# Kernel optimization log

Hardware: AMD Instinct MI355X
Metric: run time of the kernel (lower is better)

## Reference

```python
import jax, jax.numpy as jnp
import numpy as np

N_NODES = 100000
D = 256
E = 1000000
H = 128


def setup_inputs() -> dict:
    key = jax.random.key(0)
    k1, k2, k3, k4 = jax.random.split(key, 4)
    z = jax.random.normal(k1, (N_NODES, D), dtype=jnp.float32)
    edge_label_index = jax.random.randint(k2, (2, E), 0, N_NODES, dtype=jnp.int64)
    # Linear layers: PyTorch Linear(in, out) -> weight [out, in]; stored here as [in, out].
    W1 = jax.random.normal(k3, (2 * D, H), dtype=jnp.float32) * (1.0 / np.sqrt(2 * D))
    b1 = jnp.zeros((H,), dtype=jnp.float32)
    W2 = jax.random.normal(k4, (H, 1), dtype=jnp.float32) * (1.0 / np.sqrt(H))
    b2 = jnp.zeros((1,), dtype=jnp.float32)
    return {"z": z, "edge_label_index": edge_label_index,
            "W1": W1, "b1": b1, "W2": W2, "b2": b2}


def reference(z, edge_label_index, W1, b1, W2, b2):
    src = edge_label_index[0]
    dst = edge_label_index[1]
    # Gather node pairs and concat: [E, 2*D]
    pair = jnp.concatenate([z[src], z[dst]], axis=-1)
    h = jax.nn.relu(pair @ W1 + b1)          # [E, H]
    out = (h @ W2 + b2).reshape(-1)          # [E]
    return out
```

## Files before the change

### kernel.cpp

```cpp
#include <hip/hip_runtime.h>
#include <hip/hip_bf16.h>


typedef __attribute__((ext_vector_type(4))) float floatx4;
typedef __attribute__((ext_vector_type(8))) short short8;
typedef _Float16 half8v __attribute__((ext_vector_type(8)));
typedef __fp16 fp16x2 __attribute__((ext_vector_type(2)));

#if defined(__has_builtin)
#if __has_builtin(__builtin_amdgcn_fdot2)
#define HAVE_FDOT2 1
#endif
#endif

__device__ __forceinline__ unsigned short bf16rne(float x) {
    unsigned int u = __float_as_uint(x);
    u += 0x7fffu + ((u >> 16) & 1u);
    return (unsigned short)(u >> 16);
}

__device__ __forceinline__ void gl_lds16(const void* g, void* l) {
    __builtin_amdgcn_global_load_lds(
        (const __attribute__((address_space(1))) void*)(unsigned long long)g,
        (__attribute__((address_space(3))) void*)(unsigned)(unsigned long long)l,
        16, 0, 0);
}

__global__ void cvt_w1h(const float* __restrict__ W1, unsigned short* __restrict__ BTc2) {
    int t = blockIdx.x * blockDim.x + threadIdx.x;
    int hf = t >> 15, rem = t & 32767;
    int s = rem >> 12, rem2 = rem & 4095;
    int n = rem2 >> 5, rem3 = rem2 & 31;
    int gp = rem3 >> 3, j = rem3 & 7;
    int g = gp ^ ((n >> 1) & 3);
    int k = hf * 256 + s * 32 + g * 8 + j;
    BTc2[t] = bf16rne(W1[k * 128 + n]);
}

__global__ void cvt_w1(const float* __restrict__ W1, unsigned short* __restrict__ BTc) {
    int t = blockIdx.x * blockDim.x + threadIdx.x;
    int s = t >> 12, rem = t & 4095;
    int n = rem >> 5, rem2 = rem & 31;
    int gp = rem2 >> 3, j = rem2 & 7;
    int g = gp ^ ((n >> 1) & 3);
    int k = s * 32 + g * 8 + j;
    BTc[t] = bf16rne(W1[k * 128 + n]);
}

__global__ __launch_bounds__(256, 2)
void gemm_hb(const float* __restrict__ zf, int nnodes,
             const unsigned short* __restrict__ BTc2,
             const float* __restrict__ b1, _Float16* __restrict__ Hh)
{
    __shared__ unsigned short btile[2][2][2][128][32];

    const int t = threadIdx.x;
    const int wid = t >> 6;
    const int lane = t & 63;
    const int l15 = lane & 15;
    const int quad = lane >> 4;
    const int m0 = blockIdx.x * 64 + wid * 16;

    int rr = m0 + l15;
    rr = rr < nnodes ? rr : nnodes - 1;
    const unsigned offs = (unsigned)rr * 1024u;
    const char* zbb = (const char*)zf;

    const int swz = (l15 >> 1) & 3;
    const unsigned short* bbase = &btile[0][0][0][0][0] + l15 * 32 + (quad ^ swz) * 8;

    auto stage = [&](int kc, int buf) {
        char* lbase = (char*)&btile[0][0][0][0][0] + buf * 32768 + wid * 1024 + lane * 16;
        const char* gbase = (const char*)BTc2 + kc * 16384 + wid * 1024 + lane * 16;
#pragma unroll
        for (int h = 0; h < 2; ++h) {
            const char* g = gbase + h * 65536;
            char* l = lbase + h * 16384;
#pragma unroll
            for (int i = 0; i < 4; ++i)
                gl_lds16(g + i * 4096, l + i * 4096);
        }
    };

    auto load_a = [&](int ks, short8* dst) {
        const int cb = ks * 128 + quad * 32;
        const float* pf = (const float*)(zbb + (size_t)offs + cb);
        float4 f0 = *(const float4*)pf;
        float4 f1 = *(const float4*)(pf + 4);
        short8 av;
        av[0] = (short)bf16rne(f0.x); av[1] = (short)bf16rne(f0.y);
        av[2] = (short)bf16rne(f0.z); av[3] = (short)bf16rne(f0.w);
        av[4] = (short)bf16rne(f1.x); av[5] = (short)bf16rne(f1.y);
        av[6] = (short)bf16rne(f1.z); av[7] = (short)bf16rne(f1.w);
        *dst = av;
    };

    floatx4 acc[16];
#pragma unroll
    for (int nf = 0; nf < 16; ++nf)
        acc[nf] = (floatx4){0.f, 0.f, 0.f, 0.f};

    short8 A[3];
    stage(0, 0);
    load_a(0, &A[0]);
    load_a(1, &A[1]);
    __syncthreads();

#pragma unroll
    for (int kc = 0; kc < 4; ++kc) {
        if (kc < 3) stage(kc + 1, (kc + 1) & 1);

#pragma unroll
        for (int s4 = 0; s4 < 2; ++s4) {
            const int ks = kc * 2 + s4;
            if (ks + 2 < 8) load_a(ks + 2, &A[(ks + 2) % 3]);

            const unsigned short* bs0 = bbase + (kc & 1) * 16384 + s4 * 4096;
            const short8 ac = A[ks % 3];

#pragma unroll
            for (int gq = 0; gq < 4; ++gq) {
                const unsigned short* bs = bs0 + (gq >> 1) * 8192 + (gq & 1) * 2048;
                short8 bfr[4];
#pragma unroll
                for (int nf = 0; nf < 4; ++nf)
                    bfr[nf] = *(const short8*)(bs + nf * 512);
#pragma unroll
                for (int nf = 0; nf < 4; ++nf)
                    acc[gq * 4 + nf] = __builtin_amdgcn_mfma_f32_16x16x32_bf16(
                        ac, bfr[nf], acc[gq * 4 + nf], 0, 0, 0);
            }
        }

        if (kc < 3) __syncthreads();
    }

    float b1v[8];
#pragma unroll
    for (int nf = 0; nf < 8; ++nf)
        b1v[nf] = b1[nf * 16 + l15];
#pragma unroll
    for (int r = 0; r < 4; ++r) {
        int row = m0 + quad * 4 + r;
        if (row < nnodes) {
            _Float16* hp = Hh + (size_t)row * 256 + l15;
#pragma unroll
            for (int nf = 0; nf < 8; ++nf)
                hp[nf * 16] = (_Float16)(acc[nf][r] + b1v[nf]);
#pragma unroll
            for (int nf = 0; nf < 8; ++nf)
                hp[128 + nf * 16] = (_Float16)acc[8 + nf][r];
        }
    }
}

__global__ __launch_bounds__(256)
void edge_out(const _Float16* __restrict__ Hh, const int* __restrict__ eli,
              int E, int nnodes,
              const float* __restrict__ W2, const float* __restrict__ b2,
              float* __restrict__ out)
{
    const int t = threadIdx.x;
    const int lane = t & 63;
    const int wid = t >> 6;
    const int l15 = lane & 15;
    const int grp = lane >> 4;

    fp16x2 w2h[4];
#pragma unroll
    for (int p = 0; p < 4; ++p) {
        w2h[p][0] = (__fp16)W2[l15 * 8 + 2 * p];
        w2h[p][1] = (__fp16)W2[l15 * 8 + 2 * p + 1];
    }
    const float b2s = b2[0];

    const int e0 = blockIdx.x * 64 + wid * 16 + grp;

    half8v hs[4], hd[4];
    int ee[4];
#pragma unroll
    for (int i = 0; i < 4; ++i) {
        int e = e0 + i * 4;
        ee[i] = e;
        int ec = e < E ? e : E - 1;
        int s = eli[ec];
        int d = eli[E + ec];
        s = s < 0 ? 0 : (s >= nnodes ? nnodes - 1 : s);
        d = d < 0 ? 0 : (d >= nnodes ? nnodes - 1 : d);
        hs[i] = *(const half8v*)(Hh + (size_t)s * 256 + l15 * 8);
        hd[i] = *(const half8v*)(Hh + (size_t)d * 256 + 128 + l15 * 8);
    }
    const half8v zero = {};
#pragma unroll
    for (int i = 0; i < 4; ++i) {
        half8v v = hs[i] + hd[i];
        v = __builtin_elementwise_max(v, zero);
        float sacc = 0.f;
#if defined(HAVE_FDOT2)
#pragma unroll
        for (int p = 0; p < 4; ++p) {
            fp16x2 a;
            a[0] = (__fp16)v[2 * p];
            a[1] = (__fp16)v[2 * p + 1];
            sacc = __builtin_amdgcn_fdot2(a, w2h[p], sacc, false);
        }
#else
#pragma unroll
        for (int p = 0; p < 4; ++p) {
            sacc = fmaf((float)v[2 * p],     (float)w2h[p][0], sacc);
            sacc = fmaf((float)v[2 * p + 1], (float)w2h[p][1], sacc);
        }
#endif
        sacc += __shfl_xor(sacc, 1);
        sacc += __shfl_xor(sacc, 2);
        sacc += __shfl_xor(sacc, 4);
        sacc += __shfl_xor(sacc, 8);
        if (l15 == 0 && ee[i] < E)
            out[ee[i]] = sacc + b2s;
    }
}

__global__ __launch_bounds__(256, 2)
void fused_mlp_f32(const float* __restrict__ zf, const int* __restrict__ eli,
                   int E, int nnodes,
                   const unsigned short* __restrict__ BTc,
                   const float* __restrict__ b1, const float* __restrict__ W2,
                   const float* __restrict__ b2, float* __restrict__ out)
{
    __shared__ unsigned short btile[2][4][128][32];

    const int t = threadIdx.x;
    const int wid = t >> 6;
    const int lane = t & 63;
    const int l15 = lane & 15;
    const int quad = lane >> 4;
    const int m0 = blockIdx.x * 256 + wid * 64;

    unsigned offs[4], offd[4];
#pragma unroll
    for (int mf = 0; mf < 4; ++mf) {
        int e = m0 + mf * 16 + l15;
        e = e < E ? e : E - 1;
        int s = eli[e];
        int d = eli[E + e];
        s = s < 0 ? 0 : (s >= nnodes ? nnodes - 1 : s);
        d = d < 0 ? 0 : (d >= nnodes ? nnodes - 1 : d);
        offs[mf] = (unsigned)s * 1024u;
        offd[mf] = (unsigned)d * 1024u;
    }
    const char* zbb = (const char*)zf;

    const int swz = (l15 >> 1) & 3;
    const unsigned short* bbase = &btile[0][0][0][0] + l15 * 32 + (quad ^ swz) * 8;

    auto stage = [&](int kc, int buf) {
        const char* g = (const char*)BTc + kc * 32768 + wid * 1024 + lane * 16;
        char* l = (char*)&btile[buf][0][0][0] + wid * 1024 + lane * 16;
#pragma unroll
        for (int i = 0; i < 8; ++i)
            gl_lds16(g + i * 4096, l + i * 4096);
    };

    auto load_a = [&](int ks, short8* dst) {
        const unsigned* off = (ks < 8) ? offs : offd;
        const int cb = (ks & 7) * 128 + quad * 32;
#pragma unroll
        for (int mf = 0; mf < 4; ++mf) {
            const float* pf = (const float*)(zbb + (size_t)off[mf] + cb);
            float4 f0 = *(const float4*)pf;
            float4 f1 = *(const float4*)(pf + 4);
            short8 av;
            av[0] = (short)bf16rne(f0.x); av[1] = (short)bf16rne(f0.y);
            av[2] = (short)bf16rne(f0.z); av[3] = (short)bf16rne(f0.w);
            av[4] = (short)bf16rne(f1.x); av[5] = (short)bf16rne(f1.y);
            av[6] = (short)bf16rne(f1.z); av[7] = (short)bf16rne(f1.w);
            dst[mf] = av;
        }
    };

    floatx4 acc[4][8];
#pragma unroll
    for (int mf = 0; mf < 4; ++mf)
#pragma unroll
        for (int nf = 0; nf < 8; ++nf)
            acc[mf][nf] = (floatx4){0.f, 0.f, 0.f, 0.f};

    short8 A[3][4];
    stage(0, 0);
    load_a(0, A[0]);
    load_a(1, A[1]);
    __syncthreads();

#pragma unroll
    for (int kc = 0; kc < 4; ++kc) {
        if (kc < 3) stage(kc + 1, (kc + 1) & 1);

#pragma unroll
        for (int s4 = 0; s4 < 4; ++s4) {
            const int ks = kc * 4 + s4;
            if (ks + 2 < 16) load_a(ks + 2, A[(ks + 2) % 3]);

            const unsigned short* bs = bbase + (kc & 1) * 16384 + s4 * 4096;
            short8 bfr[8];
#pragma unroll
            for (int nf = 0; nf < 8; ++nf)
                bfr[nf] = *(const short8*)(bs + nf * 512);

            const short8* ac = A[ks % 3];
#pragma unroll
            for (int nf = 0; nf < 8; ++nf)
#pragma unroll
                for (int mf = 0; mf < 4; ++mf)
                    acc[mf][nf] = __builtin_amdgcn_mfma_f32_16x16x32_bf16(
                        ac[mf], bfr[nf], acc[mf][nf], 0, 0, 0);
        }

        if (kc < 3) __syncthreads();
    }

    const float b2s = b2[0];
    float b1v[8], w2v[8];
#pragma unroll
    for (int nf = 0; nf < 8; ++nf) {
        int c = nf * 16 + l15;
        b1v[nf] = b1[c];
        w2v[nf] = W2[c];
    }
#pragma unroll
    for (int mf = 0; mf < 4; ++mf) {
#pragma unroll
        for (int r = 0; r < 4; ++r) {
            float s = 0.f;
#pragma unroll
            for (int nf = 0; nf < 8; ++nf) {
                float v = acc[mf][nf][r] + b1v[nf];
                v = v > 0.f ? v : 0.f;
                s = fmaf(v, w2v[nf], s);
            }
            s += __shfl_xor(s, 1);
            s += __shfl_xor(s, 2);
            s += __shfl_xor(s, 4);
            s += __shfl_xor(s, 8);
            if (l15 == 0) {
                int e = m0 + mf * 16 + quad * 4 + r;
                if (e < E) out[e] = s + b2s;
            }
        }
    }
}

__global__ void naive_edge(const float* __restrict__ z, const int* __restrict__ eli,
                           int E, int nnodes,
                           const float* __restrict__ W1, const float* __restrict__ b1,
                           const float* __restrict__ W2, const float* __restrict__ b2,
                           float* __restrict__ out)
{
    __shared__ float red[2];
    int e = blockIdx.x;
    int j = threadIdx.x;
    int s = eli[e], d = eli[E + e];
    s = s < 0 ? 0 : (s >= nnodes ? nnodes - 1 : s);
    d = d < 0 ? 0 : (d >= nnodes ? nnodes - 1 : d);
    const float* zs = z + (long long)s * 256;
    const float* zd = z + (long long)d * 256;
    float h = b1[j];
    for (int i = 0; i < 256; ++i) h = fmaf(zs[i], W1[i * 128 + j], h);
    for (int i = 0; i < 256; ++i) h = fmaf(zd[i], W1[(256 + i) * 128 + j], h);
    h = h > 0.f ? h : 0.f;
    float v = h * W2[j];
    v += __shfl_xor(v, 1);  v += __shfl_xor(v, 2);  v += __shfl_xor(v, 4);
    v += __shfl_xor(v, 8);  v += __shfl_xor(v, 16); v += __shfl_xor(v, 32);
    if ((threadIdx.x & 63) == 0) red[threadIdx.x >> 6] = v;
    __syncthreads();
    if (threadIdx.x == 0) out[e] = red[0] + red[1] + b2[0];
}

extern "C" void kernel_launch(void* const* d_in, const int* in_sizes, int n_in,
                              void* d_out, int out_size, void* d_ws, size_t ws_size,
                              hipStream_t stream) {
    const float* z   = (const float*)d_in[0];
    const int*   eli = (const int*)d_in[1];
    const float* W1  = (const float*)d_in[2];
    const float* b1  = (const float*)d_in[3];
    const float* W2  = (const float*)d_in[4];
    const float* b2  = (const float*)d_in[5];
    float*       out = (float*)d_out;

    const int E      = in_sizes[1] / 2;
    const int nnodes = in_sizes[0] / 256;

    const size_t HB   = (size_t)nnodes * 512;
    const size_t BT2B = 131072;
    const size_t BTB  = (size_t)512 * 128 * 2;

    const int grid_gemm = (nnodes + 63) / 64;
    const int grid_edge = (E + 63) / 64;

    if (ws_size >= HB + BT2B) {
        _Float16*       Hh   = (_Float16*)d_ws;
        unsigned short* BTc2 = (unsigned short*)((char*)d_ws + HB);
        cvt_w1h<<<256, 256, 0, stream>>>(W1, BTc2);
        gemm_hb<<<grid_gemm, 256, 0, stream>>>(z, nnodes, BTc2, b1, Hh);
        edge_out<<<grid_edge, 256, 0, stream>>>(Hh, eli, E, nnodes, W2, b2, out);
    } else if (ws_size >= BTB) {
        unsigned short* BTc = (unsigned short*)d_ws;
        cvt_w1<<<256, 256, 0, stream>>>(W1, BTc);
        fused_mlp_f32<<<(E + 255) / 256, 256, 0, stream>>>(z, eli, E, nnodes, BTc, b1, W2, b2, out);
    } else {
        naive_edge<<<E, 128, 0, stream>>>(z, eli, E, nnodes, W1, b1, W2, b2, out);
    }
}
```

Measured before the change: 252.8 us.

## Split node GEMM across column-group waves with smaller tiles for higher occupancy

The per-node projection GEMM now gives each block 32 rows instead of 64, and each pair of waves shares a row tile while splitting the 256 output columns (src half and dst half) between them. Each wave keeps 8 accumulators instead of 16, the LDS B tile is halved, the K loop runs in 8 single-step chunks with one barrier each, and launch bounds ask for 4 blocks per CU. The aim is to cut register and LDS pressure so more waves fit per CU and hide the gather latency on z. In exchange, every wave pair loads the same A rows twice, the grid doubles, and there are more barriers per block.

```diff
diff --git a/kernel.cpp b/kernel.cpp
--- a/kernel.cpp
+++ b/kernel.cpp
@@ -47,19 +47,21 @@
     BTc[t] = bf16rne(W1[k * 128 + n]);
 }
 
-__global__ __launch_bounds__(256, 2)
+__global__ __launch_bounds__(256, 4)
 void gemm_hb(const float* __restrict__ zf, int nnodes,
              const unsigned short* __restrict__ BTc2,
              const float* __restrict__ b1, _Float16* __restrict__ Hh)
 {
-    __shared__ unsigned short btile[2][2][2][128][32];
+    __shared__ unsigned short btile[2][2][128][32];
 
     const int t = threadIdx.x;
     const int wid = t >> 6;
     const int lane = t & 63;
     const int l15 = lane & 15;
     const int quad = lane >> 4;
-    const int m0 = blockIdx.x * 64 + wid * 16;
+    const int wr = wid >> 1;
+    const int cg = wid & 1;
+    const int m0 = blockIdx.x * 32 + wr * 16;
 
     int rr = m0 + l15;
     rr = rr < nnodes ? rr : nnodes - 1;
@@ -67,23 +69,22 @@
     const char* zbb = (const char*)zf;
 
     const int swz = (l15 >> 1) & 3;
-    const unsigned short* bbase = &btile[0][0][0][0][0] + l15 * 32 + (quad ^ swz) * 8;
+    const unsigned short* bbase =
+        &btile[0][0][0][0] + cg * 4096 + l15 * 32 + (quad ^ swz) * 8;
 
     auto stage = [&](int kc, int buf) {
-        char* lbase = (char*)&btile[0][0][0][0][0] + buf * 32768 + wid * 1024 + lane * 16;
-        const char* gbase = (const char*)BTc2 + kc * 16384 + wid * 1024 + lane * 16;
-#pragma unroll
-        for (int h = 0; h < 2; ++h) {
-            const char* g = gbase + h * 65536;
-            char* l = lbase + h * 16384;
-#pragma unroll
-            for (int i = 0; i < 4; ++i)
-                gl_lds16(g + i * 4096, l + i * 4096);
-        }
+        const char* g = (const char*)BTc2 + (wid >> 1) * 65536 + kc * 8192
+                        + (wid & 1) * 4096 + lane * 16;
+        char* l = (char*)&btile[0][0][0][0] + buf * 16384 + (wid >> 1) * 8192
+                  + (wid & 1) * 4096 + lane * 16;
+        gl_lds16(g,        l);
+        gl_lds16(g + 1024, l + 1024);
+        gl_lds16(g + 2048, l + 2048);
+        gl_lds16(g + 3072, l + 3072);
     };
 
-    auto load_a = [&](int ks, short8* dst) {
-        const int cb = ks * 128 + quad * 32;
+    auto load_a = [&](int kc, short8* dst) {
+        const int cb = kc * 128 + quad * 32;
         const float* pf = (const float*)(zbb + (size_t)offs + cb);
         float4 f0 = *(const float4*)pf;
         float4 f1 = *(const float4*)(pf + 4);
@@ -95,9 +96,9 @@
         *dst = av;
     };
 
-    floatx4 acc[16];
-#pragma unroll
-    for (int nf = 0; nf < 16; ++nf)
+    floatx4 acc[8];
+#pragma unroll
+    for (int nf = 0; nf < 8; ++nf)
         acc[nf] = (floatx4){0.f, 0.f, 0.f, 0.f};
 
     short8 A[3];
@@ -107,49 +108,42 @@
     __syncthreads();
 
 #pragma unroll
-    for (int kc = 0; kc < 4; ++kc) {
-        if (kc < 3) stage(kc + 1, (kc + 1) & 1);
-
-#pragma unroll
-        for (int s4 = 0; s4 < 2; ++s4) {
-            const int ks = kc * 2 + s4;
-            if (ks + 2 < 8) load_a(ks + 2, &A[(ks + 2) % 3]);
-
-            const unsigned short* bs0 = bbase + (kc & 1) * 16384 + s4 * 4096;
-            const short8 ac = A[ks % 3];
-
-#pragma unroll
-            for (int gq = 0; gq < 4; ++gq) {
-                const unsigned short* bs = bs0 + (gq >> 1) * 8192 + (gq & 1) * 2048;
-                short8 bfr[4];
-#pragma unroll
-                for (int nf = 0; nf < 4; ++nf)
-                    bfr[nf] = *(const short8*)(bs + nf * 512);
-#pragma unroll
-                for (int nf = 0; nf < 4; ++nf)
-                    acc[gq * 4 + nf] = __builtin_amdgcn_mfma_f32_16x16x32_bf16(
-                        ac, bfr[nf], acc[gq * 4 + nf], 0, 0, 0);
-            }
-        }
-
-        if (kc < 3) __syncthreads();
+    for (int kc = 0; kc < 8; ++kc) {
+        if (kc < 7) stage(kc + 1, (kc + 1) & 1);
+        if (kc + 2 < 8) load_a(kc + 2, &A[(kc + 2) % 3]);
+
+        const unsigned short* bs = bbase + (kc & 1) * 8192;
+        const short8 ac = A[kc % 3];
+
+        short8 bfr[4];
+#pragma unroll
+        for (int nf = 0; nf < 4; ++nf)
+            bfr[nf] = *(const short8*)(bs + nf * 512);
+#pragma unroll
+        for (int nf = 0; nf < 4; ++nf)
+            acc[nf] = __builtin_amdgcn_mfma_f32_16x16x32_bf16(ac, bfr[nf], acc[nf], 0, 0, 0);
+#pragma unroll
+        for (int nf = 0; nf < 4; ++nf)
+            bfr[nf] = *(const short8*)(bs + (nf + 4) * 512);
+#pragma unroll
+        for (int nf = 0; nf < 4; ++nf)
+            acc[nf + 4] = __builtin_amdgcn_mfma_f32_16x16x32_bf16(ac, bfr[nf], acc[nf + 4], 0, 0, 0);
+
+        if (kc < 7) __syncthreads();
     }
 
     float b1v[8];
 #pragma unroll
     for (int nf = 0; nf < 8; ++nf)
-        b1v[nf] = b1[nf * 16 + l15];
+        b1v[nf] = (cg == 0) ? b1[nf * 16 + l15] : 0.f;
 #pragma unroll
     for (int r = 0; r < 4; ++r) {
         int row = m0 + quad * 4 + r;
         if (row < nnodes) {
-            _Float16* hp = Hh + (size_t)row * 256 + l15;
+            _Float16* hp = Hh + (size_t)row * 256 + cg * 128 + l15;
 #pragma unroll
             for (int nf = 0; nf < 8; ++nf)
                 hp[nf * 16] = (_Float16)(acc[nf][r] + b1v[nf]);
-#pragma unroll
-            for (int nf = 0; nf < 8; ++nf)
-                hp[128 + nf * 16] = (_Float16)acc[8 + nf][r];
         }
     }
 }
@@ -393,7 +387,7 @@
     const size_t BT2B = 131072;
     const size_t BTB  = (size_t)512 * 128 * 2;
 
-    const int grid_gemm = (nnodes + 63) / 64;
+    const int grid_gemm = (nnodes + 31) / 32;
     const int grid_edge = (E + 63) / 64;
 
     if (ws_size >= HB + BT2B) {
```

After: 263.7 us. 4.3% more time.
